# Kernel optimization log

Measured on AMD Instinct MI355X. Metric: run time of the kernel, lower is better.

The kernel has to match this reference:

```python
import jax, jax.numpy as jnp
import numpy as np

HEADS = 8
DIM_HEAD = 64


def setup_inputs() -> dict:
    key = jax.random.key(0)
    ks = jax.random.split(key, 10)
    B, NQ, NK, D, INNER = 4, 2048, 2048, 1024, HEADS * DIM_HEAD
    w_scale = 0.02
    return {
        "x": jax.random.normal(ks[0], (B, NQ, D), jnp.float32),
        "context": jax.random.normal(ks[1], (B, NK, D), jnp.float32),
        "wq": jax.random.normal(ks[2], (D, INNER), jnp.float32) * w_scale,
        "bq": jax.random.normal(ks[3], (INNER,), jnp.float32) * w_scale,
        "wk": jax.random.normal(ks[4], (D, INNER), jnp.float32) * w_scale,
        "bk": jax.random.normal(ks[5], (INNER,), jnp.float32) * w_scale,
        "wv": jax.random.normal(ks[6], (D, INNER), jnp.float32) * w_scale,
        "bv": jax.random.normal(ks[7], (INNER,), jnp.float32) * w_scale,
        "wo": jax.random.normal(ks[8], (INNER, D), jnp.float32) * w_scale,
        "bo": jax.random.normal(ks[9], (D,), jnp.float32) * w_scale,
    }


def _split_heads(t):
    # [b, n, h*d] -> [b, h, n, d]
    b, n, _ = t.shape
    return t.reshape(b, n, HEADS, DIM_HEAD).transpose(0, 2, 1, 3)


def reference(x, context, wq, bq, wk, bk, wv, bv, wo, bo):
    scale = DIM_HEAD ** -0.5
    q = _split_heads(x @ wq + bq)        # [b, h, nq, d]
    k = _split_heads(context @ wk + bk)  # [b, h, nk, d]
    v = _split_heads(context @ wv + bv)  # [b, h, nk, d]
    sim = jnp.einsum('bhid,bhjd->bhij', q, k) * scale  # full score matrix, as in original
    attn = jax.nn.softmax(sim, axis=-1)
    out = jnp.einsum('bhij,bhjd->bhid', attn, v)       # [b, h, nq, d]
    b, h, n, d = out.shape
    out = out.transpose(0, 2, 1, 3).reshape(b, n, h * d)
    return out @ wo + bo
```

## Files before the change

### kernel.cpp

```cpp
#include <hip/hip_runtime.h>
#include <hip/hip_bf16.h>

typedef __attribute__((ext_vector_type(8))) short short8;
typedef __attribute__((ext_vector_type(4))) float f32x4;

__device__ __forceinline__ short f2bf(float f) {
  union { float f; unsigned u; } x; x.f = f;
  unsigned r = x.u + 0x7fffu + ((x.u >> 16) & 1u);
  return (short)(r >> 16);
}

__device__ __forceinline__ void gload16(const short* g, short* l) {
  __builtin_amdgcn_global_load_lds(
      (const __attribute__((address_space(1))) unsigned*)g,
      (__attribute__((address_space(3))) unsigned*)l, 16, 0, 0);
}

__global__ void cast_bf16_kernel(const float* __restrict__ src,
                                 short* __restrict__ dst, int n) {
  int i = (blockIdx.x * 256 + threadIdx.x) * 4;
  if (i < n) {
    float4 f = *(const float4*)(src + i);
    union { short s[4]; uint2 u; } o;
    o.s[0] = f2bf(f.x); o.s[1] = f2bf(f.y);
    o.s[2] = f2bf(f.z); o.s[3] = f2bf(f.w);
    *(uint2*)(dst + i) = o.u;
  }
}

__global__ __launch_bounds__(256) void transpose_cast_kernel(
    const float* __restrict__ src, short* __restrict__ dst, int R, int C) {
  __shared__ short tile[64][72];
  int tpc = C >> 6;
  int bx = blockIdx.x % tpc, by = blockIdx.x / tpc;
  int r0 = by * 64, c0 = bx * 64;
  int tx = threadIdx.x & 15, ty = threadIdx.x >> 4;
#pragma unroll
  for (int i = 0; i < 4; i++) {
    int r = i * 16 + ty;
    float4 f = *(const float4*)(src + (size_t)(r0 + r) * C + c0 + tx * 4);
    union { short s[4]; uint2 u; } o;
    o.s[0] = f2bf(f.x); o.s[1] = f2bf(f.y);
    o.s[2] = f2bf(f.z); o.s[3] = f2bf(f.w);
    *(uint2*)&tile[r][tx * 4] = o.u;
  }
  __syncthreads();
#pragma unroll
  for (int i = 0; i < 4; i++) {
    int c = i * 16 + ty;
    union { short s[4]; uint2 u; } o;
#pragma unroll
    for (int k = 0; k < 4; k++) o.s[k] = tile[tx * 4 + k][c];
    *(uint2*)(dst + (size_t)(c0 + c) * R + r0 + tx * 4) = o.u;
  }
}

__device__ __forceinline__ void gemm_core(
    const short* __restrict__ A, const short* __restrict__ Bt, int K,
    int mblk, int nblk, short* sA, short* sB, f32x4 (&acc)[4][4]) {
  int tid = threadIdx.x;
  int lane = tid & 63, wave = tid >> 6;
  int quad = lane >> 4, l15 = lane & 15;
  int wm = (wave >> 1) * 64, wn = (wave & 1) * 64;
  int sub = lane >> 3, e8 = lane & 7;
  int swz = (e8 ^ sub) << 3;
  int s0 = (quad ^ (l15 & 7)) << 3;
  const short* Ag = A + (size_t)(mblk + 32 * wave + sub) * K + swz;
  const short* Bg = Bt + (size_t)(nblk + 32 * wave + sub) * K + swz;
  short* Al = sA + 4 * wave * 512;
  short* Bl = sB + 4 * wave * 512;

  for (int k0 = 0; k0 < K; k0 += 64) {
    __syncthreads();
#pragma unroll
    for (int t = 0; t < 4; t++) {
      gload16(Ag + (size_t)(8 * t) * K + k0, Al + t * 512);
      gload16(Bg + (size_t)(8 * t) * K + k0, Bl + t * 512);
    }
    __syncthreads();
#pragma unroll
    for (int h = 0; h < 2; h++) {
      int so = s0 ^ (h << 5);
      short8 af[4], bf[4];
#pragma unroll
      for (int mt = 0; mt < 4; mt++)
        af[mt] = *(const short8*)(&sA[(wm + mt * 16 + l15) * 64 + so]);
#pragma unroll
      for (int nt = 0; nt < 4; nt++)
        bf[nt] = *(const short8*)(&sB[(wn + nt * 16 + l15) * 64 + so]);
#pragma unroll
      for (int mt = 0; mt < 4; mt++)
#pragma unroll
        for (int nt = 0; nt < 4; nt++)
          acc[mt][nt] = __builtin_amdgcn_mfma_f32_16x16x32_bf16(
              af[mt], bf[nt], acc[mt][nt], 0, 0, 0);
    }
  }
}

__global__ __launch_bounds__(256) void gemm_qkv(
    const short* __restrict__ xb, const short* __restrict__ cb,
    const short* __restrict__ wqt, const short* __restrict__ wkt,
    const short* __restrict__ wvt,
    const float* __restrict__ bq, const float* __restrict__ bk,
    const float* __restrict__ bv,
    short* __restrict__ Qb, short* __restrict__ Kb, short* __restrict__ Vt) {
  __shared__ __align__(16) short sA[128 * 64];
  __shared__ __align__(16) short sB[128 * 64];
  int z = blockIdx.z;
  const short* A  = (z == 0) ? xb : cb;
  const short* Bt = (z == 0) ? wqt : (z == 1) ? wkt : wvt;
  const float* bias = (z == 0) ? bq : (z == 1) ? bk : bv;
  short* out = (z == 0) ? Qb : (z == 1) ? Kb : Vt;
  float scale = (z == 0) ? 0.18033688011112042f : 1.0f;
  int mblk = blockIdx.x * 128, nblk = blockIdx.y * 128;
  f32x4 acc[4][4] = {};
  gemm_core(A, Bt, 1024, mblk, nblk, sA, sB, acc);

  int lane = threadIdx.x & 63, wave = threadIdx.x >> 6;
  int quad = lane >> 4, l15 = lane & 15;
  int wm = (wave >> 1) * 64, wn = (wave & 1) * 64;
#pragma unroll
  for (int nt = 0; nt < 4; nt++) {
    int col = nblk + wn + nt * 16 + l15;
    float bias_v = bias[col];
    int h = col >> 6, dh = col & 63;
#pragma unroll
    for (int mt = 0; mt < 4; mt++)
#pragma unroll
      for (int r = 0; r < 4; r++) {
        int row = mblk + wm + mt * 16 + quad * 4 + r;
        float v = (acc[mt][nt][r] + bias_v) * scale;
        int b = row >> 11, n = row & 2047;
        size_t base = ((size_t)(b * 8 + h)) << 17;
        size_t idx = (z == 2) ? base + ((size_t)dh << 11) + n
                              : base + ((size_t)n << 6) + dh;
        out[idx] = f2bf(v);
      }
  }
}

__global__ __launch_bounds__(256) void gemm_out(
    const short* __restrict__ Ob, const short* __restrict__ wot,
    const float* __restrict__ bo, float* __restrict__ out) {
  __shared__ __align__(16) short sA[128 * 64];
  __shared__ __align__(16) short sB[128 * 64];
  int mblk = blockIdx.x * 128, nblk = blockIdx.y * 128;
  f32x4 acc[4][4] = {};
  gemm_core(Ob, wot, 512, mblk, nblk, sA, sB, acc);
  int lane = threadIdx.x & 63, wave = threadIdx.x >> 6;
  int quad = lane >> 4, l15 = lane & 15;
  int wm = (wave >> 1) * 64, wn = (wave & 1) * 64;
#pragma unroll
  for (int nt = 0; nt < 4; nt++) {
    int col = nblk + wn + nt * 16 + l15;
    float bias_v = bo[col];
#pragma unroll
    for (int mt = 0; mt < 4; mt++)
#pragma unroll
      for (int r = 0; r < 4; r++) {
        int row = mblk + wm + mt * 16 + quad * 4 + r;
        out[(size_t)row * 1024 + col] = acc[mt][nt][r] + bias_v;
      }
  }
}

__global__ __launch_bounds__(256, 4) void attn_kernel(
    const short* __restrict__ Qb, const short* __restrict__ Kb,
    const short* __restrict__ Vt, short* __restrict__ Ob) {
  __shared__ __align__(16) short sK[64 * 64];
  __shared__ __align__(16) short sV[64 * 64];
  __shared__ __align__(16) unsigned sP[4][640];
  int tid = threadIdx.x;
  int lane = tid & 63, wave = tid >> 6;
  int quad = lane >> 4, l15 = lane & 15;
  int bh = blockIdx.x & 31, qt = blockIdx.x >> 5;
  const short* Qp = Qb + ((size_t)bh << 17);
  const short* Kp = Kb + ((size_t)bh << 17);
  const short* Vp = Vt + ((size_t)bh << 17);
  int qrow0 = qt * 64 + wave * 16;
  short8 qf0 = *(const short8*)(Qp + (size_t)(qrow0 + l15) * 64 + quad * 8);
  short8 qf1 = *(const short8*)(Qp + (size_t)(qrow0 + l15) * 64 + 32 + quad * 8);

  int jk0 = 2 * wave, jk1 = 2 * wave + 1;
  int sub = lane >> 3;
  int e8  = lane & 7;
  int swz = (e8 ^ sub) << 3;
  const short* kg0 = Kp + (size_t)(8 * jk0 + sub) * 64 + e8 * 8;
  const short* kg1 = Kp + (size_t)(8 * jk1 + sub) * 64 + e8 * 8;
  short* kl0 = &sK[(8 * jk0 + sub) * 64 + swz];
  short* kl1 = &sK[(8 * jk1 + sub) * 64 + swz];
  const short* vg0 = Vp + (size_t)(8 * jk0 + sub) * 2048 + e8 * 8;
  const short* vg1 = Vp + (size_t)(8 * jk1 + sub) * 2048 + e8 * 8;
  short* vl0 = &sV[(8 * jk0 + sub) * 64 + swz];
  short* vl1 = &sV[(8 * jk1 + sub) * 64 + swz];

  int s0 = (quad ^ (l15 & 7)) << 3;
  int s1 = s0 ^ 32;

  f32x4 o[4] = {};
  float lsum = 0.f;
  unsigned* pw = &sP[wave][0];

  uint4 rk0 = *(const uint4*)kg0, rk1 = *(const uint4*)kg1;
  uint4 rv0 = *(const uint4*)vg0, rv1 = *(const uint4*)vg1;

  for (int it = 0; it < 32; ++it) {
    __syncthreads();
    *(uint4*)kl0 = rk0; *(uint4*)kl1 = rk1;
    *(uint4*)vl0 = rv0; *(uint4*)vl1 = rv1;
    if (it < 31) {
      int off = (it + 1) * 64;
      rk0 = *(const uint4*)(kg0 + (size_t)off * 64);
      rk1 = *(const uint4*)(kg1 + (size_t)off * 64);
      rv0 = *(const uint4*)(vg0 + off);
      rv1 = *(const uint4*)(vg1 + off);
    }
    __syncthreads();
    f32x4 st[4];
#pragma unroll
    for (int jt = 0; jt < 4; jt++) {
      short8 k0 = *(const short8*)(&sK[(jt * 16 + l15) * 64 + s0]);
      short8 k1 = *(const short8*)(&sK[(jt * 16 + l15) * 64 + s1]);
      f32x4 zz = {0.f, 0.f, 0.f, 0.f};
      zz = __builtin_amdgcn_mfma_f32_16x16x32_bf16(k0, qf0, zz, 0, 0, 0);
      st[jt] = __builtin_amdgcn_mfma_f32_16x16x32_bf16(k1, qf1, zz, 0, 0, 0);
    }
#pragma unroll
    for (int jt = 0; jt < 4; jt++) {
      float p0 = exp2f(st[jt][0]), p1 = exp2f(st[jt][1]);
      float p2 = exp2f(st[jt][2]), p3 = exp2f(st[jt][3]);
      lsum += (p0 + p1) + (p2 + p3);
      union { __hip_bfloat162 b; unsigned u; } a0, a1;
      a0.b = __float22bfloat162_rn(make_float2(p0, p1));
      a1.b = __float22bfloat162_rn(make_float2(p2, p3));
      int kpair = 8 * jt + 2 * quad;
      pw[(kpair + 0) * 20 + l15] = a0.u;
      pw[(kpair + 1) * 20 + l15] = a1.u;
    }
    union { unsigned u[4]; short8 s; } P0, P1;
#pragma unroll
    for (int c = 0; c < 4; c++) {
      P0.u[c] = pw[(4 * quad + c) * 20 + l15];
      P1.u[c] = pw[(16 + 4 * quad + c) * 20 + l15];
    }
#pragma unroll
    for (int nt = 0; nt < 4; nt++) {
      short8 v0 = *(const short8*)(&sV[(nt * 16 + l15) * 64 + s0]);
      short8 v1 = *(const short8*)(&sV[(nt * 16 + l15) * 64 + s1]);
      o[nt] = __builtin_amdgcn_mfma_f32_16x16x32_bf16(v0, P0.s, o[nt], 0, 0, 0);
      o[nt] = __builtin_amdgcn_mfma_f32_16x16x32_bf16(v1, P1.s, o[nt], 0, 0, 0);
    }
  }
  lsum += __shfl_xor(lsum, 16, 64);
  lsum += __shfl_xor(lsum, 32, 64);
  float inv = 1.0f / lsum;
  int b = bh >> 3, h = bh & 7;
  size_t rowbase = ((size_t)b * 2048 + qrow0 + l15) * 512 + h * 64 + quad * 4;
#pragma unroll
  for (int nt = 0; nt < 4; nt++) {
    union { short s[4]; uint2 u; } pk2;
#pragma unroll
    for (int r = 0; r < 4; r++) pk2.s[r] = f2bf(o[nt][r] * inv);
    *(uint2*)(Ob + rowbase + nt * 16) = pk2.u;
  }
}

extern "C" void kernel_launch(void* const* d_in, const int* in_sizes, int n_in,
                              void* d_out, int out_size, void* d_ws, size_t ws_size,
                              hipStream_t stream) {
  const float* x   = (const float*)d_in[0];
  const float* ctx = (const float*)d_in[1];
  const float* wq  = (const float*)d_in[2];
  const float* bq  = (const float*)d_in[3];
  const float* wk  = (const float*)d_in[4];
  const float* bk  = (const float*)d_in[5];
  const float* wv  = (const float*)d_in[6];
  const float* bv  = (const float*)d_in[7];
  const float* wo  = (const float*)d_in[8];
  const float* bo  = (const float*)d_in[9];
  float* out = (float*)d_out;
  char* ws = (char*)d_ws;

  short* xb  = (short*)(ws);
  short* cb  = (short*)(ws + (16ull << 20));
  short* wqt = (short*)(ws + (32ull << 20));
  short* wkt = (short*)(ws + (33ull << 20));
  short* wvt = (short*)(ws + (34ull << 20));
  short* wot = (short*)(ws + (35ull << 20));
  short* Qb  = (short*)(ws + (36ull << 20));
  short* Kb  = (short*)(ws + (44ull << 20));
  short* Vt  = (short*)(ws + (52ull << 20));
  short* Ob  = (short*)(ws + (60ull << 20));

  cast_bf16_kernel<<<8192, 256, 0, stream>>>(x, xb, 1 << 23);
  cast_bf16_kernel<<<8192, 256, 0, stream>>>(ctx, cb, 1 << 23);
  transpose_cast_kernel<<<128, 256, 0, stream>>>(wq, wqt, 1024, 512);
  transpose_cast_kernel<<<128, 256, 0, stream>>>(wk, wkt, 1024, 512);
  transpose_cast_kernel<<<128, 256, 0, stream>>>(wv, wvt, 1024, 512);
  transpose_cast_kernel<<<128, 256, 0, stream>>>(wo, wot, 512, 1024);
  gemm_qkv<<<dim3(64, 4, 3), 256, 0, stream>>>(xb, cb, wqt, wkt, wvt,
                                               bq, bk, bv, Qb, Kb, Vt);
  attn_kernel<<<1024, 256, 0, stream>>>(Qb, Kb, Vt, Ob);
  gemm_out<<<dim3(64, 8), 256, 0, stream>>>(Ob, wot, bo, out);
}
```

Before: 261.2 us.

## Split keys across waves in attention and add separate V transpose kernel

The attention kernel now has each wave process all 64 query rows against its own 32-key slice of a 128-key tile. This lets each K and V fragment loaded from LDS be reused across four query groups. Partial outputs and row sums are combined at the end through a shared-memory tree reduction across waves, and occupancy drops to 2 blocks per CU. The QKV GEMM now writes V row-major instead of scattering transposed stores, and a new vtrans_kernel transposes V through LDS, at the cost of one extra launch and an extra round trip of V through memory.

```diff
diff --git a/kernel.cpp b/kernel.cpp
--- a/kernel.cpp
+++ b/kernel.cpp
@@ -52,6 +52,34 @@
 #pragma unroll
     for (int k = 0; k < 4; k++) o.s[k] = tile[tx * 4 + k][c];
     *(uint2*)(dst + (size_t)(c0 + c) * R + r0 + tx * 4) = o.u;
+  }
+}
+
+__global__ __launch_bounds__(256) void vtrans_kernel(
+    const short* __restrict__ Vb, short* __restrict__ Vt) {
+  __shared__ short tile[64 * 73 + 8];
+  int t = threadIdx.x;
+  int bh = blockIdx.x & 31, ntile = blockIdx.x >> 5;
+  const short* src = Vb + ((size_t)bh << 17) + (size_t)ntile * 64 * 64;
+  short* dst = Vt + ((size_t)bh << 17) + ntile * 64;
+#pragma unroll
+  for (int i = 0; i < 2; i++) {
+    int lin = t + 256 * i;
+    int row = lin >> 3, u = lin & 7;
+    union { short s[8]; uint4 v; } d;
+    d.v = *(const uint4*)(src + row * 64 + u * 8);
+#pragma unroll
+    for (int j = 0; j < 8; j++) tile[row * 73 + u * 8 + j] = d.s[j];
+  }
+  __syncthreads();
+#pragma unroll
+  for (int i = 0; i < 2; i++) {
+    int lin = t + 256 * i;
+    int dh = lin >> 3, u = lin & 7;
+    union { short s[8]; uint4 v; } d;
+#pragma unroll
+    for (int j = 0; j < 8; j++) d.s[j] = tile[(8 * u + j) * 73 + dh];
+    *(uint4*)(dst + (size_t)dh * 2048 + 8 * u) = d.v;
   }
 }
 
@@ -104,14 +132,14 @@
     const short* __restrict__ wvt,
     const float* __restrict__ bq, const float* __restrict__ bk,
     const float* __restrict__ bv,
-    short* __restrict__ Qb, short* __restrict__ Kb, short* __restrict__ Vt) {
+    short* __restrict__ Qb, short* __restrict__ Kb, short* __restrict__ Vb) {
   __shared__ __align__(16) short sA[128 * 64];
   __shared__ __align__(16) short sB[128 * 64];
   int z = blockIdx.z;
   const short* A  = (z == 0) ? xb : cb;
   const short* Bt = (z == 0) ? wqt : (z == 1) ? wkt : wvt;
   const float* bias = (z == 0) ? bq : (z == 1) ? bk : bv;
-  short* out = (z == 0) ? Qb : (z == 1) ? Kb : Vt;
+  short* out = (z == 0) ? Qb : (z == 1) ? Kb : Vb;
   float scale = (z == 0) ? 0.18033688011112042f : 1.0f;
   int mblk = blockIdx.x * 128, nblk = blockIdx.y * 128;
   f32x4 acc[4][4] = {};
@@ -132,9 +160,7 @@
         int row = mblk + wm + mt * 16 + quad * 4 + r;
         float v = (acc[mt][nt][r] + bias_v) * scale;
         int b = row >> 11, n = row & 2047;
-        size_t base = ((size_t)(b * 8 + h)) << 17;
-        size_t idx = (z == 2) ? base + ((size_t)dh << 11) + n
-                              : base + ((size_t)n << 6) + dh;
+        size_t idx = (((size_t)(b * 8 + h)) << 17) + ((size_t)n << 6) + dh;
         out[idx] = f2bf(v);
       }
   }
@@ -165,12 +191,13 @@
   }
 }
 
-__global__ __launch_bounds__(256, 4) void attn_kernel(
+__global__ __launch_bounds__(256, 2) void attn_kernel(
     const short* __restrict__ Qb, const short* __restrict__ Kb,
     const short* __restrict__ Vt, short* __restrict__ Ob) {
-  __shared__ __align__(16) short sK[64 * 64];
-  __shared__ __align__(16) short sV[64 * 64];
-  __shared__ __align__(16) unsigned sP[4][640];
+  __shared__ __align__(16) short smem[26624];
+  short* sK = smem;
+  short* sV = smem + 8192;
+  unsigned* sP = (unsigned*)(smem + 16384);
   int tid = threadIdx.x;
   int lane = tid & 63, wave = tid >> 6;
   int quad = lane >> 4, l15 = lane & 15;
@@ -178,91 +205,152 @@
   const short* Qp = Qb + ((size_t)bh << 17);
   const short* Kp = Kb + ((size_t)bh << 17);
   const short* Vp = Vt + ((size_t)bh << 17);
-  int qrow0 = qt * 64 + wave * 16;
-  short8 qf0 = *(const short8*)(Qp + (size_t)(qrow0 + l15) * 64 + quad * 8);
-  short8 qf1 = *(const short8*)(Qp + (size_t)(qrow0 + l15) * 64 + 32 + quad * 8);
-
-  int jk0 = 2 * wave, jk1 = 2 * wave + 1;
-  int sub = lane >> 3;
-  int e8  = lane & 7;
-  int swz = (e8 ^ sub) << 3;
-  const short* kg0 = Kp + (size_t)(8 * jk0 + sub) * 64 + e8 * 8;
-  const short* kg1 = Kp + (size_t)(8 * jk1 + sub) * 64 + e8 * 8;
-  short* kl0 = &sK[(8 * jk0 + sub) * 64 + swz];
-  short* kl1 = &sK[(8 * jk1 + sub) * 64 + swz];
-  const short* vg0 = Vp + (size_t)(8 * jk0 + sub) * 2048 + e8 * 8;
-  const short* vg1 = Vp + (size_t)(8 * jk1 + sub) * 2048 + e8 * 8;
-  short* vl0 = &sV[(8 * jk0 + sub) * 64 + swz];
-  short* vl1 = &sV[(8 * jk1 + sub) * 64 + swz];
-
-  int s0 = (quad ^ (l15 & 7)) << 3;
-  int s1 = s0 ^ 32;
-
-  f32x4 o[4] = {};
-  float lsum = 0.f;
-  unsigned* pw = &sP[wave][0];
-
-  uint4 rk0 = *(const uint4*)kg0, rk1 = *(const uint4*)kg1;
-  uint4 rv0 = *(const uint4*)vg0, rv1 = *(const uint4*)vg1;
-
-  for (int it = 0; it < 32; ++it) {
+  int qrow0 = qt * 64;
+  short8 qf[4][2];
+#pragma unroll
+  for (int g = 0; g < 4; g++)
+#pragma unroll
+    for (int h = 0; h < 2; h++)
+      qf[g][h] = *(const short8*)(Qp + (size_t)(qrow0 + 16 * g + l15) * 64 +
+                                  32 * h + quad * 8);
+  f32x4 o[4][4] = {};
+  float lsum[4] = {0.f, 0.f, 0.f, 0.f};
+
+  int sub = lane >> 3, e8 = lane & 7;
+  int sub4 = lane >> 4, u16 = lane & 15;
+  const short* kgb = Kp + (size_t)(32 * wave + sub) * 64 + e8 * 8;
+  short* klb = sK + (32 * wave + sub) * 64 + ((e8 ^ sub) << 3);
+  const short* vgb = Vp + (size_t)(16 * wave + sub4) * 2048 + u16 * 8;
+  short* vlb = sV + (16 * wave + sub4) * 128;
+  unsigned* pPw = sP + wave * 1280;
+
+  uint4 rk[4], rv[4];
+#pragma unroll
+  for (int t = 0; t < 4; t++) {
+    rk[t] = *(const uint4*)(kgb + (size_t)(8 * t) * 64);
+    rv[t] = *(const uint4*)(vgb + (size_t)(4 * t) * 2048);
+  }
+
+  for (int it = 0; it < 16; ++it) {
     __syncthreads();
-    *(uint4*)kl0 = rk0; *(uint4*)kl1 = rk1;
-    *(uint4*)vl0 = rv0; *(uint4*)vl1 = rv1;
-    if (it < 31) {
-      int off = (it + 1) * 64;
-      rk0 = *(const uint4*)(kg0 + (size_t)off * 64);
-      rk1 = *(const uint4*)(kg1 + (size_t)off * 64);
-      rv0 = *(const uint4*)(vg0 + off);
-      rv1 = *(const uint4*)(vg1 + off);
+#pragma unroll
+    for (int t = 0; t < 4; t++) {
+      *(uint4*)(klb + 8 * t * 64) = rk[t];
+      *(uint4*)(vlb + 4 * t * 128 + ((u16 ^ ((4 * t + sub4) & 15)) << 3)) = rv[t];
+    }
+    if (it < 15) {
+      int kb = (it + 1) * 128;
+#pragma unroll
+      for (int t = 0; t < 4; t++) {
+        rk[t] = *(const uint4*)(kgb + (size_t)(kb + 8 * t) * 64);
+        rv[t] = *(const uint4*)(vgb + (size_t)(4 * t) * 2048 + kb);
+      }
     }
     __syncthreads();
-    f32x4 st[4];
-#pragma unroll
-    for (int jt = 0; jt < 4; jt++) {
-      short8 k0 = *(const short8*)(&sK[(jt * 16 + l15) * 64 + s0]);
-      short8 k1 = *(const short8*)(&sK[(jt * 16 + l15) * 64 + s1]);
-      f32x4 zz = {0.f, 0.f, 0.f, 0.f};
-      zz = __builtin_amdgcn_mfma_f32_16x16x32_bf16(k0, qf0, zz, 0, 0, 0);
-      st[jt] = __builtin_amdgcn_mfma_f32_16x16x32_bf16(k1, qf1, zz, 0, 0, 0);
-    }
-#pragma unroll
-    for (int jt = 0; jt < 4; jt++) {
-      float p0 = exp2f(st[jt][0]), p1 = exp2f(st[jt][1]);
-      float p2 = exp2f(st[jt][2]), p3 = exp2f(st[jt][3]);
-      lsum += (p0 + p1) + (p2 + p3);
-      union { __hip_bfloat162 b; unsigned u; } a0, a1;
-      a0.b = __float22bfloat162_rn(make_float2(p0, p1));
-      a1.b = __float22bfloat162_rn(make_float2(p2, p3));
-      int kpair = 8 * jt + 2 * quad;
-      pw[(kpair + 0) * 20 + l15] = a0.u;
-      pw[(kpair + 1) * 20 + l15] = a1.u;
-    }
-    union { unsigned u[4]; short8 s; } P0, P1;
-#pragma unroll
-    for (int c = 0; c < 4; c++) {
-      P0.u[c] = pw[(4 * quad + c) * 20 + l15];
-      P1.u[c] = pw[(16 + 4 * quad + c) * 20 + l15];
-    }
-#pragma unroll
-    for (int nt = 0; nt < 4; nt++) {
-      short8 v0 = *(const short8*)(&sV[(nt * 16 + l15) * 64 + s0]);
-      short8 v1 = *(const short8*)(&sV[(nt * 16 + l15) * 64 + s1]);
-      o[nt] = __builtin_amdgcn_mfma_f32_16x16x32_bf16(v0, P0.s, o[nt], 0, 0, 0);
-      o[nt] = __builtin_amdgcn_mfma_f32_16x16x32_bf16(v1, P1.s, o[nt], 0, 0, 0);
-    }
-  }
-  lsum += __shfl_xor(lsum, 16, 64);
-  lsum += __shfl_xor(lsum, 32, 64);
-  float inv = 1.0f / lsum;
-  int b = bh >> 3, h = bh & 7;
-  size_t rowbase = ((size_t)b * 2048 + qrow0 + l15) * 512 + h * 64 + quad * 4;
-#pragma unroll
-  for (int nt = 0; nt < 4; nt++) {
-    union { short s[4]; uint2 u; } pk2;
-#pragma unroll
-    for (int r = 0; r < 4; r++) pk2.s[r] = f2bf(o[nt][r] * inv);
-    *(uint2*)(Ob + rowbase + nt * 16) = pk2.u;
+    short8 kf[2][2];
+#pragma unroll
+    for (int a = 0; a < 2; a++)
+#pragma unroll
+      for (int h = 0; h < 2; h++)
+        kf[a][h] = *(const short8*)(
+            &sK[(32 * wave + 16 * a + l15) * 64 +
+                ((((h << 2) | quad) ^ (l15 & 7)) << 3)]);
+#pragma unroll
+    for (int a = 0; a < 2; a++)
+#pragma unroll
+      for (int g = 0; g < 4; g++) {
+        f32x4 st = {0.f, 0.f, 0.f, 0.f};
+        st = __builtin_amdgcn_mfma_f32_16x16x32_bf16(kf[a][0], qf[g][0], st, 0, 0, 0);
+        st = __builtin_amdgcn_mfma_f32_16x16x32_bf16(kf[a][1], qf[g][1], st, 0, 0, 0);
+        float p0 = exp2f(st[0]), p1 = exp2f(st[1]);
+        float p2 = exp2f(st[2]), p3 = exp2f(st[3]);
+        lsum[g] += (p0 + p1) + (p2 + p3);
+        union { __hip_bfloat162 b; unsigned u; } a0, a1;
+        a0.b = __float22bfloat162_rn(make_float2(p0, p1));
+        a1.b = __float22bfloat162_rn(make_float2(p2, p3));
+        uint2 w; w.x = a0.u; w.y = a1.u;
+        *(uint2*)(pPw + (16 * g + l15) * 20 + 8 * a + 2 * quad) = w;
+      }
+    union { unsigned u[4]; short8 s; } pf[4];
+#pragma unroll
+    for (int g = 0; g < 4; g++)
+      *(uint4*)pf[g].u = *(const uint4*)(pPw + (16 * g + l15) * 20 + 4 * quad);
+    short8 vf[4];
+#pragma unroll
+    for (int nt = 0; nt < 4; nt++)
+      vf[nt] = *(const short8*)(
+          &sV[(16 * nt + l15) * 128 + (((4 * wave + quad) ^ l15) << 3)]);
+#pragma unroll
+    for (int nt = 0; nt < 4; nt++)
+#pragma unroll
+      for (int g = 0; g < 4; g++)
+        o[nt][g] = __builtin_amdgcn_mfma_f32_16x16x32_bf16(
+            vf[nt], pf[g].s, o[nt][g], 0, 0, 0);
+  }
+
+#pragma unroll
+  for (int g = 0; g < 4; g++) {
+    lsum[g] += __shfl_xor(lsum[g], 16, 64);
+    lsum[g] += __shfl_xor(lsum[g], 32, 64);
+  }
+  float* redO = (float*)smem;
+  float* redL = (float*)smem + 8704;
+  __syncthreads();
+  if (wave >= 2) {
+    float* d = redO + (wave - 2) * 4352 + lane * 68;
+#pragma unroll
+    for (int nt = 0; nt < 4; nt++)
+#pragma unroll
+      for (int g = 0; g < 4; g++)
+        *(f32x4*)(d + nt * 16 + g * 4) = o[nt][g];
+    if (quad == 0)
+#pragma unroll
+      for (int g = 0; g < 4; g++) redL[(wave - 2) * 64 + g * 16 + l15] = lsum[g];
+  }
+  __syncthreads();
+  if (wave < 2) {
+    float* s = redO + wave * 4352 + lane * 68;
+#pragma unroll
+    for (int nt = 0; nt < 4; nt++)
+#pragma unroll
+      for (int g = 0; g < 4; g++) {
+        f32x4 v = *(const f32x4*)(s + nt * 16 + g * 4);
+#pragma unroll
+        for (int r = 0; r < 4; r++) o[nt][g][r] += v[r];
+      }
+#pragma unroll
+    for (int g = 0; g < 4; g++) lsum[g] += redL[wave * 64 + g * 16 + l15];
+  }
+  __syncthreads();
+  if (wave == 1) {
+    float* d = redO + lane * 68;
+#pragma unroll
+    for (int nt = 0; nt < 4; nt++)
+#pragma unroll
+      for (int g = 0; g < 4; g++)
+        *(f32x4*)(d + nt * 16 + g * 4) = o[nt][g];
+    if (quad == 0)
+#pragma unroll
+      for (int g = 0; g < 4; g++) redL[g * 16 + l15] = lsum[g];
+  }
+  __syncthreads();
+  if (wave == 0) {
+    float* s = redO + lane * 68;
+    int b = bh >> 3, h = bh & 7;
+#pragma unroll
+    for (int g = 0; g < 4; g++) {
+      float inv = 1.0f / (lsum[g] + redL[g * 16 + l15]);
+      size_t rowbase = ((size_t)b * 2048 + qrow0 + 16 * g + l15) * 512 +
+                       h * 64 + 4 * quad;
+#pragma unroll
+      for (int nt = 0; nt < 4; nt++) {
+        f32x4 v = *(const f32x4*)(s + nt * 16 + g * 4);
+        union { short sh[4]; uint2 u; } pk;
+#pragma unroll
+        for (int r = 0; r < 4; r++) pk.sh[r] = f2bf((o[nt][g][r] + v[r]) * inv);
+        *(uint2*)(Ob + rowbase + 16 * nt) = pk.u;
+      }
+    }
   }
 }
 
@@ -292,6 +380,7 @@
   short* Kb  = (short*)(ws + (44ull << 20));
   short* Vt  = (short*)(ws + (52ull << 20));
   short* Ob  = (short*)(ws + (60ull << 20));
+  short* Vb  = Ob;
 
   cast_bf16_kernel<<<8192, 256, 0, stream>>>(x, xb, 1 << 23);
   cast_bf16_kernel<<<8192, 256, 0, stream>>>(ctx, cb, 1 << 23);
@@ -300,7 +389,8 @@
   transpose_cast_kernel<<<128, 256, 0, stream>>>(wv, wvt, 1024, 512);
   transpose_cast_kernel<<<128, 256, 0, stream>>>(wo, wot, 512, 1024);
   gemm_qkv<<<dim3(64, 4, 3), 256, 0, stream>>>(xb, cb, wqt, wkt, wvt,
-                                               bq, bk, bv, Qb, Kb, Vt);
+                                               bq, bk, bv, Qb, Kb, Vb);
+  vtrans_kernel<<<1024, 256, 0, stream>>>(Vb, Vt);
   attn_kernel<<<1024, 256, 0, stream>>>(Qb, Kb, Vt, Ob);
   gemm_out<<<dim3(64, 8), 256, 0, stream>>>(Ob, wot, bo, out);
 }
```

Measured after the change: 369.0 us. 41.3% more time.
